# Kernel tuning notes

Measured on AMD Instinct MI355X. Metric: run time of the kernel, lower is better.

## Reference

```python
import jax, jax.numpy as jnp
import numpy as np

N = 50000      # nodes
E = 400000     # edges
F_IN = 128     # num_features
HID = 64       # hidden_channels
HEADS = 4      # num_heads
HEADC = HID // HEADS  # 16
C = 10         # num_classes
K_HOPS = 2     # K
CST = 1e-05


def setup_inputs() -> dict:
    key = jax.random.key(0)
    ks = jax.random.split(key, 12)
    def lin(k, out_dim, in_dim):
        return jax.random.normal(k, (out_dim, in_dim), jnp.float32) / np.sqrt(in_dim).astype(np.float32)
    return {
        "node_feat": jax.random.normal(ks[0], (N, F_IN), jnp.float32),
        "edge_index": jax.random.randint(ks[1], (2, E), 0, N, jnp.int64),
        "W_in": lin(ks[2], HID, F_IN),   "b_in": jnp.zeros((HID,), jnp.float32),
        "W_q": lin(ks[3], HEADS * HEADC, HID), "b_q": jnp.zeros((HEADS * HEADC,), jnp.float32),
        "W_k": lin(ks[4], HEADS * HEADC, HID), "b_k": jnp.zeros((HEADS * HEADC,), jnp.float32),
        "W_v": lin(ks[5], HEADS * C, HID),     "b_v": jnp.zeros((HEADS * C,), jnp.float32),
        "W_out": lin(ks[6], C, HEADS * C),     "b_out": jnp.zeros((C,), jnp.float32),
        "hopwise": jnp.ones((K_HOPS + 1,), jnp.float32),
        "headwise": jnp.zeros((HEADS, K_HOPS), jnp.float32),
    }


def reference(node_feat, edge_index, W_in, b_in, W_q, b_q, W_k, b_k, W_v, b_v,
              W_out, b_out, hopwise, headwise):
    # input transform (dropout is identity in eval mode)
    x = jax.nn.relu(node_feat @ W_in.T + b_in)                       # [N, HID]
    Q = (1.0 + jax.nn.elu(x @ W_q.T + b_q)).reshape(N, HEADS, HEADC)  # [N,H,hc]
    Kf = (1.0 + jax.nn.elu(x @ W_k.T + b_k)).reshape(N, HEADS, HEADC)
    V = (x @ W_v.T + b_v).reshape(N, HEADS, C)                        # [N,H,C]

    M = jnp.einsum('nhi,nhj->nhij', Kf, V)                            # [N,H,hc,C]
    hidden = V * hopwise[0]                                           # gamma_softmax path
    layerwise = jax.nn.softmax(headwise, axis=0)                      # softmax over heads

    row, col = edge_index[0], edge_index[1]
    for hop in range(K_HOPS):
        # propM / propK: sum-aggregate source features into targets
        M = jax.ops.segment_sum(M[row], col, num_segments=N)
        Kf = jax.ops.segment_sum(Kf[row], col, num_segments=N)
        H = jnp.einsum('nhi,nhij->nhj', Q, M)                         # [N,H,C]
        Cd = jnp.einsum('nhi,nhi->nh', Q, Kf)[..., None] + CST        # [N,H,1]
        gamma = hopwise[hop + 1] * layerwise[:, hop][:, None]         # [H,1]
        hidden = hidden + gamma * (H / Cd)

    # multi_concat output projection
    out = hidden.reshape(N, HEADS * C) @ W_out.T + b_out              # [N,C]
    return out
```

## Files before the change

kernel.cpp:

```cpp
#include <hip/hip_runtime.h>
#include <hip/hip_bf16.h>

#define N_NODES 50000
#define N_EDGES 400000
#define F_IN    128
#define HID     64
#define HEADS   4
#define HEADC   16
#define C_CLS   10
#define HC      (HEADS * C_CLS)
#define CST     1e-5f

#define WIN_OFF 0
#define WQ_OFF  1024
#define WK_OFF  1536
#define WV_OFF  2048
#define WB_TOT  2432

typedef short bf16x8 __attribute__((ext_vector_type(8)));
typedef float f32x4  __attribute__((ext_vector_type(4)));
typedef float floatx2 __attribute__((ext_vector_type(2)));

__device__ __forceinline__ unsigned pack_bf16x2(float a, float b) {
    union { __hip_bfloat162 h2; unsigned u; } cv;
    cv.h2.x = __float2bfloat16(a);
    cv.h2.y = __float2bfloat16(b);
    return cv.u;
}
__device__ __forceinline__ float2 bf2_to_f2(unsigned u) {
    union { unsigned x; float f; } a, b;
    a.x = u << 16;
    b.x = u & 0xffff0000u;
    return make_float2(a.f, b.f);
}
union FragU { uint4 u; bf16x8 b; };
__device__ __forceinline__ bf16x8 ldfrag(const uint4* p) { FragU f; f.u = *p; return f.b; }
__device__ __forceinline__ bf16x8 pack8(const float4& a0, const float4& a1) {
    FragU f;
    f.u.x = pack_bf16x2(a0.x, a0.y);
    f.u.y = pack_bf16x2(a0.z, a0.w);
    f.u.z = pack_bf16x2(a1.x, a1.y);
    f.u.w = pack_bf16x2(a1.z, a1.w);
    return f.b;
}

__global__ __launch_bounds__(256) void prep_kernel(
    const float* __restrict__ W_in, const float* __restrict__ W_q,
    const float* __restrict__ W_k,  const float* __restrict__ W_v,
    uint4* __restrict__ WB)
{
    const int idx = blockIdx.x * 256 + threadIdx.x;
    if (idx >= WB_TOT) return;
    const int lane = idx & 63;
    const int c = lane & 15, g = lane >> 4;
    const float* src = nullptr;
    if (idx < WQ_OFF) {
        const int f = idx >> 6, nt = f >> 2, kt = f & 3;
        src = W_in + (size_t)(nt * 16 + c) * F_IN + kt * 32 + g * 8;
    } else if (idx < WK_OFF) {
        const int f = (idx - WQ_OFF) >> 6, nt = f >> 1, kt = f & 1;
        src = W_q + (size_t)(nt * 16 + c) * HID + kt * 32 + g * 8;
    } else if (idx < WV_OFF) {
        const int f = (idx - WK_OFF) >> 6, nt = f >> 1, kt = f & 1;
        src = W_k + (size_t)(nt * 16 + c) * HID + kt * 32 + g * 8;
    } else {
        const int f = (idx - WV_OFF) >> 6, nt = f >> 1, kt = f & 1;
        const int row = nt * 16 + c;
        src = (row < HC) ? (W_v + (size_t)row * HID + kt * 32 + g * 8) : nullptr;
    }
    float v[8];
    #pragma unroll
    for (int j = 0; j < 8; ++j) v[j] = src ? src[j] : 0.0f;
    uint4 o;
    o.x = pack_bf16x2(v[0], v[1]);
    o.y = pack_bf16x2(v[2], v[3]);
    o.z = pack_bf16x2(v[4], v[5]);
    o.w = pack_bf16x2(v[6], v[7]);
    WB[idx] = o;
}

__global__ __launch_bounds__(256) void proj_kernel(
    const float* __restrict__ feat, const uint4* __restrict__ WB,
    const float* __restrict__ b_in, const float* __restrict__ b_q,
    const float* __restrict__ b_k,  const float* __restrict__ b_v,
    float* __restrict__ Q, __hip_bfloat16* __restrict__ Kf0,
    __hip_bfloat16* __restrict__ V0p)
{
    const int w = threadIdx.x >> 6;
    const int l = threadIdx.x & 63;
    const int c = l & 15, g = l >> 4;
    const int nb = blockIdx.x * 64 + w * 16;
    __shared__ float xs[4][16][68];

    f32x4 acc[4];
    #pragma unroll
    for (int nt = 0; nt < 4; ++nt) acc[nt] = (f32x4){0.f, 0.f, 0.f, 0.f};
    int arow = nb + c; if (arow >= N_NODES) arow = N_NODES - 1;
    const float* fbase = feat + (size_t)arow * F_IN + g * 8;
    #pragma unroll
    for (int kt = 0; kt < 4; ++kt) {
        const float4 a0 = *(const float4*)(fbase + kt * 32);
        const float4 a1 = *(const float4*)(fbase + kt * 32 + 4);
        const bf16x8 af = pack8(a0, a1);
        #pragma unroll
        for (int nt = 0; nt < 4; ++nt)
            acc[nt] = __builtin_amdgcn_mfma_f32_16x16x32_bf16(
                af, ldfrag(WB + WIN_OFF + (nt * 4 + kt) * 64 + l), acc[nt], 0, 0, 0);
    }
    #pragma unroll
    for (int nt = 0; nt < 4; ++nt) {
        const int col = nt * 16 + c;
        const float bi = b_in[col];
        #pragma unroll
        for (int i = 0; i < 4; ++i)
            xs[w][g * 4 + i][col] = fmaxf(acc[nt][i] + bi, 0.f);
    }
    __syncthreads();

    f32x4 qa[4], ka[4], va[3];
    #pragma unroll
    for (int nt = 0; nt < 4; ++nt) { qa[nt] = (f32x4){0.f,0.f,0.f,0.f}; ka[nt] = qa[nt]; }
    #pragma unroll
    for (int nt = 0; nt < 3; ++nt) va[nt] = (f32x4){0.f,0.f,0.f,0.f};
    #pragma unroll
    for (int kt = 0; kt < 2; ++kt) {
        const float* xr = &xs[w][c][kt * 32 + g * 8];
        const float4 x0 = *(const float4*)xr;
        const float4 x1 = *(const float4*)(xr + 4);
        const bf16x8 af = pack8(x0, x1);
        #pragma unroll
        for (int nt = 0; nt < 4; ++nt) {
            qa[nt] = __builtin_amdgcn_mfma_f32_16x16x32_bf16(
                af, ldfrag(WB + WQ_OFF + (nt * 2 + kt) * 64 + l), qa[nt], 0, 0, 0);
            ka[nt] = __builtin_amdgcn_mfma_f32_16x16x32_bf16(
                af, ldfrag(WB + WK_OFF + (nt * 2 + kt) * 64 + l), ka[nt], 0, 0, 0);
        }
        #pragma unroll
        for (int nt = 0; nt < 3; ++nt)
            va[nt] = __builtin_amdgcn_mfma_f32_16x16x32_bf16(
                af, ldfrag(WB + WV_OFF + (nt * 2 + kt) * 64 + l), va[nt], 0, 0, 0);
    }

    #pragma unroll
    for (int nt = 0; nt < 4; ++nt) {
        const int col = nt * 16 + c;
        const float bq = b_q[col], bk = b_k[col];
        #pragma unroll
        for (int i = 0; i < 4; ++i) {
            const int node = nb + g * 4 + i;
            if (node < N_NODES) {
                const float zq = qa[nt][i] + bq;
                Q[(size_t)node * HID + col] = (zq > 0.f) ? (zq + 1.f) : expf(zq);
                const float zk = ka[nt][i] + bk;
                Kf0[(size_t)node * HID + col] =
                    __float2bfloat16((zk > 0.f) ? (zk + 1.f) : expf(zk));
            }
        }
    }
    #pragma unroll
    for (int nt = 0; nt < 3; ++nt) {
        const int col = nt * 16 + c;
        if (col < HC) {
            const int hh = col / C_CLS, jj = col - hh * C_CLS;
            const float bv = b_v[col];
            #pragma unroll
            for (int i = 0; i < 4; ++i) {
                const int node = nb + g * 4 + i;
                if (node < N_NODES)
                    V0p[(size_t)node * 64 + hh * 16 + jj] = __float2bfloat16(va[nt][i] + bv);
            }
        }
    }
}

__global__ __launch_bounds__(256) void hist_kernel(
    const int* __restrict__ ecol, int* __restrict__ deg)
{
    const int e = blockIdx.x * 256 + threadIdx.x;
    if (e < N_EDGES) atomicAdd(&deg[ecol[e]], 1);
}

__global__ __launch_bounds__(256) void offsets_kernel(
    const int* __restrict__ deg, int* __restrict__ rowptr,
    int* __restrict__ cursor, int* __restrict__ gcount)
{
    const int t    = threadIdx.x;
    const int lane = t & 63;
    const int wid  = t >> 6;
    const int n    = blockIdx.x * 256 + t;
    const int d    = (n < N_NODES) ? deg[n] : 0;

    int x = d;
    #pragma unroll
    for (int off = 1; off < 64; off <<= 1) {
        int v = __shfl_up(x, off);
        x += (lane >= off) ? v : 0;
    }

    __shared__ int wsum[4];
    __shared__ int wbase[4];
    __shared__ int bbase;
    if (lane == 63) wsum[wid] = x;
    __syncthreads();
    if (t == 0) {
        int b = 0;
        #pragma unroll
        for (int w = 0; w < 4; ++w) { wbase[w] = b; b += wsum[w]; }
        bbase = atomicAdd(gcount, b);
    }
    __syncthreads();

    if (n < N_NODES) {
        const int excl = bbase + wbase[wid] + (x - d);
        rowptr[n] = excl;
        cursor[n] = excl;
    }
}

__global__ __launch_bounds__(256) void scatter_kernel(
    const int* __restrict__ erow, const int* __restrict__ ecol,
    int* __restrict__ cursor, int* __restrict__ csr_src)
{
    const int e = blockIdx.x * 256 + threadIdx.x;
    if (e < N_EDGES) {
        const int pos = atomicAdd(&cursor[ecol[e]], 1);
        csr_src[pos] = erow[e];
    }
}

__global__ __launch_bounds__(256) void hop1_gather(
    const int* __restrict__ csr_src, const int* __restrict__ rowptr,
    const int* __restrict__ deg,
    const float* __restrict__ Q, const __hip_bfloat16* __restrict__ Kf0,
    const __hip_bfloat16* __restrict__ V0p,
    uint2* __restrict__ M1a, unsigned* __restrict__ M1b,
    float* __restrict__ H1, float* __restrict__ Cd1)
{
    const int sub  = threadIdx.x >> 6;
    const int lane = threadIdx.x & 63;
    const int n    = blockIdx.x * 4 + sub;
    if (n >= N_NODES) return;
    const int h = lane >> 4;
    const int r = lane & 15;

    const uint4* v4 = (const uint4*)V0p;

    float accM[C_CLS];
    #pragma unroll
    for (int j = 0; j < C_CLS; ++j) accM[j] = 0.0f;
    float accK = 0.0f;

    const int beg = rowptr[n];
    const int d   = deg[n];
    int e = 0;
    for (; e + 4 <= d; e += 4) {
        int s[4];
        #pragma unroll
        for (int i = 0; i < 4; ++i) s[i] = csr_src[beg + e + i];
        float kf[4];
        uint4 va[4];
        unsigned vb[4];
        #pragma unroll
        for (int i = 0; i < 4; ++i) {
            kf[i] = __bfloat162float(Kf0[(size_t)s[i] * HID + lane]);
            const uint4* vp = v4 + (size_t)s[i] * 8 + h * 2;
            va[i] = vp[0];
            vb[i] = *(const unsigned*)(vp + 1);
        }
        accK += (kf[0] + kf[1]) + (kf[2] + kf[3]);
        #pragma unroll
        for (int i = 0; i < 4; ++i) {
            float2 f;
            f = bf2_to_f2(va[i].x); accM[0] += kf[i] * f.x; accM[1] += kf[i] * f.y;
            f = bf2_to_f2(va[i].y); accM[2] += kf[i] * f.x; accM[3] += kf[i] * f.y;
            f = bf2_to_f2(va[i].z); accM[4] += kf[i] * f.x; accM[5] += kf[i] * f.y;
            f = bf2_to_f2(va[i].w); accM[6] += kf[i] * f.x; accM[7] += kf[i] * f.y;
            f = bf2_to_f2(vb[i]);   accM[8] += kf[i] * f.x; accM[9] += kf[i] * f.y;
        }
    }
    for (; e < d; ++e) {
        const int ss = csr_src[beg + e];
        const float kf = __bfloat162float(Kf0[(size_t)ss * HID + lane]);
        const uint4* vp = v4 + (size_t)ss * 8 + h * 2;
        const uint4 va0 = vp[0];
        const unsigned vb0 = *(const unsigned*)(vp + 1);
        accK += kf;
        float2 f;
        f = bf2_to_f2(va0.x); accM[0] += kf * f.x; accM[1] += kf * f.y;
        f = bf2_to_f2(va0.y); accM[2] += kf * f.x; accM[3] += kf * f.y;
        f = bf2_to_f2(va0.z); accM[4] += kf * f.x; accM[5] += kf * f.y;
        f = bf2_to_f2(va0.w); accM[6] += kf * f.x; accM[7] += kf * f.y;
        f = bf2_to_f2(vb0);   accM[8] += kf * f.x; accM[9] += kf * f.y;
    }

    int d0 = 0, d1 = 0, d2 = 0;
    d0 = __builtin_amdgcn_cvt_pk_fp8_f32(accM[0], accM[1], d0, false);
    d0 = __builtin_amdgcn_cvt_pk_fp8_f32(accM[2], accM[3], d0, true);
    d1 = __builtin_amdgcn_cvt_pk_fp8_f32(accM[4], accM[5], d1, false);
    d1 = __builtin_amdgcn_cvt_pk_fp8_f32(accM[6], accM[7], d1, true);
    d2 = __builtin_amdgcn_cvt_pk_fp8_f32(accM[8], accM[9], d2, false);
    uint2 sa; sa.x = (unsigned)d0; sa.y = (unsigned)d1;
    M1a[(size_t)n * 64 + lane] = sa;
    M1b[(size_t)n * 64 + lane] =
        ((unsigned)d2 & 0xFFFFu) | (pack_bf16x2(0.f, accK) & 0xFFFF0000u);

    const float q = Q[(size_t)n * HID + lane];
    float pc = q * accK;
    pc += __shfl_xor(pc, 1);
    pc += __shfl_xor(pc, 2);
    pc += __shfl_xor(pc, 4);
    pc += __shfl_xor(pc, 8);
    if (r == 0) Cd1[(size_t)n * HEADS + h] = pc;

    float pj[C_CLS];
    #pragma unroll
    for (int j = 0; j < C_CLS; ++j) {
        pj[j] = q * accM[j];
        pj[j] += __shfl_xor(pj[j], 1);
        pj[j] += __shfl_xor(pj[j], 2);
        pj[j] += __shfl_xor(pj[j], 4);
        pj[j] += __shfl_xor(pj[j], 8);
    }
    if (r < C_CLS) {
        float val = 0.0f;
        #pragma unroll
        for (int j = 0; j < C_CLS; ++j) val = (r == j) ? pj[j] : val;
        H1[(size_t)n * HC + h * C_CLS + r] = val;
    }
}

__global__ __launch_bounds__(256) void hop2_gather(
    const int* __restrict__ csr_src, const int* __restrict__ rowptr,
    const int* __restrict__ deg,
    const float* __restrict__ Q,
    const uint2* __restrict__ M1a, const unsigned* __restrict__ M1b,
    float* __restrict__ H2, float* __restrict__ Cd2)
{
    const int sub  = threadIdx.x >> 6;
    const int lane = threadIdx.x & 63;
    const int n    = blockIdx.x * 4 + sub;
    if (n >= N_NODES) return;
    const int h = lane >> 4;
    const int r = lane & 15;

    const float q = Q[(size_t)n * HID + lane];
    float accM[C_CLS];
    #pragma unroll
    for (int j = 0; j < C_CLS; ++j) accM[j] = 0.0f;
    float accK = 0.0f;

    const int beg = rowptr[n];
    const int d   = deg[n];
    int e = 0;
    for (; e + 4 <= d; e += 4) {
        int s[4];
        #pragma unroll
        for (int i = 0; i < 4; ++i) s[i] = csr_src[beg + e + i];
        uint2 wa[4];
        unsigned wb[4];
        #pragma unroll
        for (int i = 0; i < 4; ++i) {
            wa[i] = M1a[(size_t)s[i] * 64 + lane];
            wb[i] = M1b[(size_t)s[i] * 64 + lane];
        }
        #pragma unroll
        for (int i = 0; i < 4; ++i) {
            accK += bf2_to_f2(wb[i]).y;
            floatx2 f;
            f = __builtin_amdgcn_cvt_pk_f32_fp8(wa[i].x, false); accM[0] += f[0]; accM[1] += f[1];
            f = __builtin_amdgcn_cvt_pk_f32_fp8(wa[i].x, true);  accM[2] += f[0]; accM[3] += f[1];
            f = __builtin_amdgcn_cvt_pk_f32_fp8(wa[i].y, false); accM[4] += f[0]; accM[5] += f[1];
            f = __builtin_amdgcn_cvt_pk_f32_fp8(wa[i].y, true);  accM[6] += f[0]; accM[7] += f[1];
            f = __builtin_amdgcn_cvt_pk_f32_fp8(wb[i], false);   accM[8] += f[0]; accM[9] += f[1];
        }
    }
    for (; e < d; ++e) {
        const int ss = csr_src[beg + e];
        const uint2 wa0 = M1a[(size_t)ss * 64 + lane];
        const unsigned wb0 = M1b[(size_t)ss * 64 + lane];
        accK += bf2_to_f2(wb0).y;
        floatx2 f;
        f = __builtin_amdgcn_cvt_pk_f32_fp8(wa0.x, false); accM[0] += f[0]; accM[1] += f[1];
        f = __builtin_amdgcn_cvt_pk_f32_fp8(wa0.x, true);  accM[2] += f[0]; accM[3] += f[1];
        f = __builtin_amdgcn_cvt_pk_f32_fp8(wa0.y, false); accM[4] += f[0]; accM[5] += f[1];
        f = __builtin_amdgcn_cvt_pk_f32_fp8(wa0.y, true);  accM[6] += f[0]; accM[7] += f[1];
        f = __builtin_amdgcn_cvt_pk_f32_fp8(wb0, false);   accM[8] += f[0]; accM[9] += f[1];
    }

    float pc = q * accK;
    pc += __shfl_xor(pc, 1);
    pc += __shfl_xor(pc, 2);
    pc += __shfl_xor(pc, 4);
    pc += __shfl_xor(pc, 8);
    if (r == 0) Cd2[(size_t)n * HEADS + h] = pc;

    float pj[C_CLS];
    #pragma unroll
    for (int j = 0; j < C_CLS; ++j) {
        pj[j] = q * accM[j];
        pj[j] += __shfl_xor(pj[j], 1);
        pj[j] += __shfl_xor(pj[j], 2);
        pj[j] += __shfl_xor(pj[j], 4);
        pj[j] += __shfl_xor(pj[j], 8);
    }
    if (r < C_CLS) {
        float val = 0.0f;
        #pragma unroll
        for (int j = 0; j < C_CLS; ++j) val = (r == j) ? pj[j] : val;
        H2[(size_t)n * HC + h * C_CLS + r] = val;
    }
}

__global__ __launch_bounds__(256) void combine_kernel(
    const __hip_bfloat16* __restrict__ V0p,
    const float* __restrict__ H1, const float* __restrict__ Cd1,
    const float* __restrict__ H2, const float* __restrict__ Cd2,
    const float* __restrict__ hopwise, const float* __restrict__ headwise,
    const float* __restrict__ W_out, const float* __restrict__ b_out,
    float* __restrict__ out)
{
    const int n = blockIdx.x * blockDim.x + threadIdx.x;
    if (n >= N_NODES) return;

    float hv[HEADS][2];
    float m0 = -1e30f, m1 = -1e30f;
    #pragma unroll
    for (int h = 0; h < HEADS; ++h) {
        hv[h][0] = headwise[h * 2 + 0];
        hv[h][1] = headwise[h * 2 + 1];
        m0 = fmaxf(m0, hv[h][0]);
        m1 = fmaxf(m1, hv[h][1]);
    }
    float s0 = 0.0f, s1 = 0.0f;
    float e0[HEADS], e1[HEADS];
    #pragma unroll
    for (int h = 0; h < HEADS; ++h) {
        e0[h] = expf(hv[h][0] - m0); s0 += e0[h];
        e1[h] = expf(hv[h][1] - m1); s1 += e1[h];
    }
    const float hw0 = hopwise[0];
    float g1[HEADS], g2[HEADS];
    #pragma unroll
    for (int h = 0; h < HEADS; ++h) {
        g1[h] = hopwise[1] * e0[h] / s0;
        g2[h] = hopwise[2] * e1[h] / s1;
    }

    float hidden[HC];
    #pragma unroll
    for (int h = 0; h < HEADS; ++h) {
        const float icd1 = 1.0f / (Cd1[(size_t)n * HEADS + h] + CST);
        const float icd2 = 1.0f / (Cd2[(size_t)n * HEADS + h] + CST);
        #pragma unroll
        for (int j = 0; j < C_CLS; ++j) {
            const int idx = h * C_CLS + j;
            hidden[idx] = hw0 * __bfloat162float(V0p[(size_t)n * 64 + h * 16 + j])
                        + g1[h] * H1[(size_t)n * HC + idx] * icd1
                        + g2[h] * H2[(size_t)n * HC + idx] * icd2;
        }
    }

    #pragma unroll
    for (int c = 0; c < C_CLS; ++c) {
        float acc = b_out[c];
        const float* w = W_out + c * HC;
        #pragma unroll
        for (int k = 0; k < HC; ++k) acc += w[k] * hidden[k];
        out[(size_t)n * C_CLS + c] = acc;
    }
}

extern "C" void kernel_launch(void* const* d_in, const int* in_sizes, int n_in,
                              void* d_out, int out_size, void* d_ws, size_t ws_size,
                              hipStream_t stream)
{
    const float* feat     = (const float*)d_in[0];
    const int*   eidx     = (const int*)  d_in[1];
    const float* W_in     = (const float*)d_in[2];
    const float* b_in     = (const float*)d_in[3];
    const float* W_q      = (const float*)d_in[4];
    const float* b_q      = (const float*)d_in[5];
    const float* W_k      = (const float*)d_in[6];
    const float* b_k      = (const float*)d_in[7];
    const float* W_v      = (const float*)d_in[8];
    const float* b_v      = (const float*)d_in[9];
    const float* W_out    = (const float*)d_in[10];
    const float* b_out    = (const float*)d_in[11];
    const float* hopwise  = (const float*)d_in[12];
    const float* headwise = (const float*)d_in[13];
    float* out = (float*)d_out;

    const int* erow = eidx;
    const int* ecol = eidx + N_EDGES;

    float* ws = (float*)d_ws;
    size_t off = 0;
    float* Q    = ws + off; off += (size_t)N_NODES * HID;
    __hip_bfloat16* Kf0 = (__hip_bfloat16*)(ws + off); off += (size_t)N_NODES * HID / 2;
    __hip_bfloat16* V0p = (__hip_bfloat16*)(ws + off); off += (size_t)N_NODES * 32;
    uint2* M1a = (uint2*)(ws + off); off += (size_t)N_NODES * 128;
    unsigned* M1b = (unsigned*)(ws + off); off += (size_t)N_NODES * 64;
    float* H1   = ws + off; off += (size_t)N_NODES * HC;
    float* Cd1  = ws + off; off += (size_t)N_NODES * HEADS;
    float* H2   = ws + off; off += (size_t)N_NODES * HC;
    float* Cd2  = ws + off; off += (size_t)N_NODES * HEADS;
    uint4* WB   = (uint4*)(ws + off); off += (size_t)WB_TOT * 4;
    int* iws = (int*)(ws + off);
    int* deg     = iws;
    int* gcount  = iws + N_NODES;
    int* rowptr  = iws + N_NODES + 1;
    int* cursor  = iws + 2 * N_NODES + 1;
    int* csr_src = iws + 3 * N_NODES + 1;

    hipMemsetAsync(deg, 0, (N_NODES + 1) * sizeof(int), stream);

    prep_kernel<<<(WB_TOT + 255) / 256, 256, 0, stream>>>(W_in, W_q, W_k, W_v, WB);

    proj_kernel<<<(N_NODES + 63) / 64, 256, 0, stream>>>(
        feat, WB, b_in, b_q, b_k, b_v, Q, Kf0, V0p);

    hist_kernel<<<(N_EDGES + 255) / 256, 256, 0, stream>>>(ecol, deg);
    offsets_kernel<<<(N_NODES + 255) / 256, 256, 0, stream>>>(deg, rowptr, cursor, gcount);
    scatter_kernel<<<(N_EDGES + 255) / 256, 256, 0, stream>>>(erow, ecol, cursor, csr_src);

    hop1_gather<<<(N_NODES + 3) / 4, 256, 0, stream>>>(
        csr_src, rowptr, deg, Q, Kf0, V0p, M1a, M1b, H1, Cd1);

    hop2_gather<<<(N_NODES + 3) / 4, 256, 0, stream>>>(
        csr_src, rowptr, deg, Q, M1a, M1b, H2, Cd2);

    combine_kernel<<<(N_NODES + 255) / 256, 256, 0, stream>>>(
        V0p, H1, Cd1, H2, Cd2, hopwise, headwise, W_out, b_out, out);
}
```

Baseline: 185.1 us.

## Gather V in fp8 via precomputed conversion and unroll hop1 gather by eight

```diff
diff --git a/kernel.cpp b/kernel.cpp
--- a/kernel.cpp
+++ b/kernel.cpp
@@ -42,6 +42,14 @@
     f.u.z = pack_bf16x2(a1.x, a1.y);
     f.u.w = pack_bf16x2(a1.z, a1.w);
     return f.b;
+}
+__device__ __forceinline__ void acc_edge_fp8(float kf, uint4 v, float* accM) {
+    floatx2 f;
+    f = __builtin_amdgcn_cvt_pk_f32_fp8(v.x, false); accM[0] += kf * f[0]; accM[1] += kf * f[1];
+    f = __builtin_amdgcn_cvt_pk_f32_fp8(v.x, true);  accM[2] += kf * f[0]; accM[3] += kf * f[1];
+    f = __builtin_amdgcn_cvt_pk_f32_fp8(v.y, false); accM[4] += kf * f[0]; accM[5] += kf * f[1];
+    f = __builtin_amdgcn_cvt_pk_f32_fp8(v.y, true);  accM[6] += kf * f[0]; accM[7] += kf * f[1];
+    f = __builtin_amdgcn_cvt_pk_f32_fp8(v.z, false); accM[8] += kf * f[0]; accM[9] += kf * f[1];
 }
 
 __global__ __launch_bounds__(256) void prep_kernel(
@@ -173,6 +181,32 @@
     }
 }
 
+__global__ __launch_bounds__(256) void vconv_kernel(
+    const __hip_bfloat16* __restrict__ V0p, uint4* __restrict__ V0f)
+{
+    const int t = blockIdx.x * 256 + threadIdx.x;
+    if (t >= N_NODES * 4) return;
+    const uint4* src = (const uint4*)V0p + (size_t)t * 2;
+    const uint4 a = src[0];
+    const unsigned b0 = ((const unsigned*)(src + 1))[0];
+    float v[10];
+    float2 f;
+    f = bf2_to_f2(a.x); v[0] = f.x; v[1] = f.y;
+    f = bf2_to_f2(a.y); v[2] = f.x; v[3] = f.y;
+    f = bf2_to_f2(a.z); v[4] = f.x; v[5] = f.y;
+    f = bf2_to_f2(a.w); v[6] = f.x; v[7] = f.y;
+    f = bf2_to_f2(b0);  v[8] = f.x; v[9] = f.y;
+    int d0 = 0, d1 = 0, d2 = 0;
+    d0 = __builtin_amdgcn_cvt_pk_fp8_f32(v[0], v[1], d0, false);
+    d0 = __builtin_amdgcn_cvt_pk_fp8_f32(v[2], v[3], d0, true);
+    d1 = __builtin_amdgcn_cvt_pk_fp8_f32(v[4], v[5], d1, false);
+    d1 = __builtin_amdgcn_cvt_pk_fp8_f32(v[6], v[7], d1, true);
+    d2 = __builtin_amdgcn_cvt_pk_fp8_f32(v[8], v[9], d2, false);
+    uint4 o;
+    o.x = (unsigned)d0; o.y = (unsigned)d1; o.z = (unsigned)d2; o.w = 0u;
+    V0f[t] = o;
+}
+
 __global__ __launch_bounds__(256) void hist_kernel(
     const int* __restrict__ ecol, int* __restrict__ deg)
 {
@@ -232,7 +266,7 @@
     const int* __restrict__ csr_src, const int* __restrict__ rowptr,
     const int* __restrict__ deg,
     const float* __restrict__ Q, const __hip_bfloat16* __restrict__ Kf0,
-    const __hip_bfloat16* __restrict__ V0p,
+    const uint4* __restrict__ V0f,
     uint2* __restrict__ M1a, unsigned* __restrict__ M1b,
     float* __restrict__ H1, float* __restrict__ Cd1)
 {
@@ -243,8 +277,6 @@
     const int h = lane >> 4;
     const int r = lane & 15;
 
-    const uint4* v4 = (const uint4*)V0p;
-
     float accM[C_CLS];
     #pragma unroll
     for (int j = 0; j < C_CLS; ++j) accM[j] = 0.0f;
@@ -253,44 +285,44 @@
     const int beg = rowptr[n];
     const int d   = deg[n];
     int e = 0;
+    for (; e + 8 <= d; e += 8) {
+        int s[8];
+        #pragma unroll
+        for (int i = 0; i < 8; ++i) s[i] = csr_src[beg + e + i];
+        float kf[8];
+        uint4 vv[8];
+        #pragma unroll
+        for (int i = 0; i < 8; ++i) {
+            kf[i] = __bfloat162float(Kf0[(size_t)s[i] * HID + lane]);
+            vv[i] = V0f[(size_t)s[i] * 4 + h];
+        }
+        #pragma unroll
+        for (int i = 0; i < 8; ++i) accK += kf[i];
+        #pragma unroll
+        for (int i = 0; i < 8; ++i) acc_edge_fp8(kf[i], vv[i], accM);
+    }
     for (; e + 4 <= d; e += 4) {
         int s[4];
         #pragma unroll
         for (int i = 0; i < 4; ++i) s[i] = csr_src[beg + e + i];
         float kf[4];
-        uint4 va[4];
-        unsigned vb[4];
+        uint4 vv[4];
         #pragma unroll
         for (int i = 0; i < 4; ++i) {
             kf[i] = __bfloat162float(Kf0[(size_t)s[i] * HID + lane]);
-            const uint4* vp = v4 + (size_t)s[i] * 8 + h * 2;
-            va[i] = vp[0];
-            vb[i] = *(const unsigned*)(vp + 1);
-        }
-        accK += (kf[0] + kf[1]) + (kf[2] + kf[3]);
-        #pragma unroll
-        for (int i = 0; i < 4; ++i) {
-            float2 f;
-            f = bf2_to_f2(va[i].x); accM[0] += kf[i] * f.x; accM[1] += kf[i] * f.y;
-            f = bf2_to_f2(va[i].y); accM[2] += kf[i] * f.x; accM[3] += kf[i] * f.y;
-            f = bf2_to_f2(va[i].z); accM[4] += kf[i] * f.x; accM[5] += kf[i] * f.y;
-            f = bf2_to_f2(va[i].w); accM[6] += kf[i] * f.x; accM[7] += kf[i] * f.y;
-            f = bf2_to_f2(vb[i]);   accM[8] += kf[i] * f.x; accM[9] += kf[i] * f.y;
-        }
+            vv[i] = V0f[(size_t)s[i] * 4 + h];
+        }
+        #pragma unroll
+        for (int i = 0; i < 4; ++i) accK += kf[i];
+        #pragma unroll
+        for (int i = 0; i < 4; ++i) acc_edge_fp8(kf[i], vv[i], accM);
     }
     for (; e < d; ++e) {
         const int ss = csr_src[beg + e];
         const float kf = __bfloat162float(Kf0[(size_t)ss * HID + lane]);
-        const uint4* vp = v4 + (size_t)ss * 8 + h * 2;
-        const uint4 va0 = vp[0];
-        const unsigned vb0 = *(const unsigned*)(vp + 1);
+        const uint4 vv0 = V0f[(size_t)ss * 4 + h];
         accK += kf;
-        float2 f;
-        f = bf2_to_f2(va0.x); accM[0] += kf * f.x; accM[1] += kf * f.y;
-        f = bf2_to_f2(va0.y); accM[2] += kf * f.x; accM[3] += kf * f.y;
-        f = bf2_to_f2(va0.z); accM[4] += kf * f.x; accM[5] += kf * f.y;
-        f = bf2_to_f2(va0.w); accM[6] += kf * f.x; accM[7] += kf * f.y;
-        f = bf2_to_f2(vb0);   accM[8] += kf * f.x; accM[9] += kf * f.y;
+        acc_edge_fp8(kf, vv0, accM);
     }
 
     int d0 = 0, d1 = 0, d2 = 0;
@@ -498,6 +530,7 @@
     float* Q    = ws + off; off += (size_t)N_NODES * HID;
     __hip_bfloat16* Kf0 = (__hip_bfloat16*)(ws + off); off += (size_t)N_NODES * HID / 2;
     __hip_bfloat16* V0p = (__hip_bfloat16*)(ws + off); off += (size_t)N_NODES * 32;
+    uint4* V0f = (uint4*)(ws + off); off += (size_t)N_NODES * 16;
     uint2* M1a = (uint2*)(ws + off); off += (size_t)N_NODES * 128;
     unsigned* M1b = (unsigned*)(ws + off); off += (size_t)N_NODES * 64;
     float* H1   = ws + off; off += (size_t)N_NODES * HC;
@@ -519,12 +552,14 @@
     proj_kernel<<<(N_NODES + 63) / 64, 256, 0, stream>>>(
         feat, WB, b_in, b_q, b_k, b_v, Q, Kf0, V0p);
 
+    vconv_kernel<<<(N_NODES * 4 + 255) / 256, 256, 0, stream>>>(V0p, V0f);
+
     hist_kernel<<<(N_EDGES + 255) / 256, 256, 0, stream>>>(ecol, deg);
     offsets_kernel<<<(N_NODES + 255) / 256, 256, 0, stream>>>(deg, rowptr, cursor, gcount);
     scatter_kernel<<<(N_EDGES + 255) / 256, 256, 0, stream>>>(erow, ecol, cursor, csr_src);
 
     hop1_gather<<<(N_NODES + 3) / 4, 256, 0, stream>>>(
-        csr_src, rowptr, deg, Q, Kf0, V0p, M1a, M1b, H1, Cd1);
+        csr_src, rowptr, deg, Q, Kf0, V0f, M1a, M1b, H1, Cd1);
 
     hop2_gather<<<(N_NODES + 3) / 4, 256, 0, stream>>>(
         csr_src, rowptr, deg, Q, M1a, M1b, H2, Cd2);
```

Measured after the change: 187.8 us. Within noise of the previous version (+1.5%).
